# Optimization experiments

Hardware: AMD Instinct MI355X
Metric: run time of the kernel (lower is better)

## Reference

```python
import jax, jax.numpy as jnp
import numpy as np

B, SRC_LEN, TRG_LEN, DIM, H, D = 64, 500, 64, 512, 1024, 6
WIN = 2 * D + 1


def setup_inputs() -> dict:
    key = jax.random.key(0)
    ks = jax.random.split(key, 18)
    p = lambda k, shape: jax.random.normal(k, shape, dtype=jnp.float32) * 0.02
    return dict(
        src=jax.random.normal(ks[0], (B, SRC_LEN, DIM), dtype=jnp.float32),
        trg=jax.random.normal(ks[1], (B, TRG_LEN, DIM), dtype=jnp.float32),
        enc_Wih=p(ks[2], (3 * H, DIM)), enc_Whh=p(ks[3], (3 * H, H)),
        enc_bih=p(ks[4], (3 * H,)), enc_bhh=p(ks[5], (3 * H,)),
        dec_Wih=p(ks[6], (3 * H, DIM + H)), dec_Whh=p(ks[7], (3 * H, H)),
        dec_bih=p(ks[8], (3 * H,)), dec_bhh=p(ks[9], (3 * H,)),
        out_W=p(ks[10], (DIM, H)), out_b=p(ks[11], (DIM,)),
        ow_W=p(ks[12], (H, H)), ow_b=p(ks[13], (H,)),
        ov_W=p(ks[14], (1, H)), ov_b=p(ks[15], (1,)),
        attn_W=p(ks[16], (H, H)), attn_b=p(ks[17], (H,)),
    )


def _gru_cell(x, h, Wih, Whh, bih, bhh):
    # torch nn.GRU cell: r,z,n gate order
    gi = x @ Wih.T + bih
    gh = h @ Whh.T + bhh
    ir, iz, inn = jnp.split(gi, 3, axis=-1)
    hr, hz, hn = jnp.split(gh, 3, axis=-1)
    r = jax.nn.sigmoid(ir + hr)
    z = jax.nn.sigmoid(iz + hz)
    n = jnp.tanh(inn + r * hn)
    return (1.0 - z) * n + z * h


def reference(src, trg, enc_Wih, enc_Whh, enc_bih, enc_bhh,
              dec_Wih, dec_Whh, dec_bih, dec_bhh,
              out_W, out_b, ow_W, ow_b, ov_W, ov_b, attn_W, attn_b):
    b, L, dim = src.shape

    # ---- encoder GRU over time ----
    h0 = jnp.zeros((b, H), src.dtype)

    def enc_step(h, x_t):
        h = _gru_cell(x_t, h, enc_Wih, enc_Whh, enc_bih, enc_bhh)
        return h, h

    hT, enc_out = jax.lax.scan(enc_step, h0, jnp.swapaxes(src, 0, 1))
    enc_out = jnp.swapaxes(enc_out, 0, 1)  # [B, L, H]

    # ---- local attention (method='general') ----
    S = float(SRC_LEN - 2 * D - 1)
    sigma = D / 2.0
    offs = jnp.arange(-D, D + 1)

    def attention(s):  # s: [B, H]
        sig_inp = (jnp.tanh(s @ ow_W.T + ow_b) @ ov_W.T + ov_b)[:, 0]  # [B]
        pt = S * jax.nn.sigmoid(sig_inp) + D  # [B], in [D, L-D-1]
        center = jnp.floor(pt).astype(jnp.int32)  # int() trunc == floor (pt>0)
        idx = center[:, None] + offs[None, :]
        window = jnp.take_along_axis(enc_out, idx[:, :, None], axis=1)
        enc_w = window @ attn_W.T + attn_b  # general: attn(enc_output)
        alpha_hat = jnp.einsum('bwh,bh->bw', enc_w, s)
        gauss = jnp.exp(-((idx.astype(s.dtype) - pt[:, None]) ** 2) / (2.0 * sigma * sigma))
        alpha = jax.nn.softmax(alpha_hat * gauss, axis=1)
        return alpha, enc_w

    # teacher forcing (ratio=1.0): dec_input at step t is trg[:, t-1], zeros at t=0
    dec_inputs = jnp.concatenate(
        [jnp.zeros((b, 1, dim), src.dtype), trg[:, :-1, :]], axis=1)
    c0 = jnp.zeros((b, H), src.dtype)

    def dec_step(carry, x_t):
        h, c = carry
        rnn_in = jnp.concatenate([x_t, c], axis=1)  # [B, DIM+H]
        h = _gru_cell(rnn_in, h, dec_Wih, dec_Whh, dec_bih, dec_bhh)
        alpha, enc_w = attention(h)
        c = jnp.einsum('bw,bwh->bh', alpha, enc_w)  # attn context
        y = h @ out_W.T + out_b  # [B, DIM]
        return (h, c), y

    _, ys = jax.lax.scan(dec_step, (hT, c0), jnp.swapaxes(dec_inputs, 0, 1))
    return jnp.swapaxes(ys, 0, 1)  # [B, TRG_LEN, DIM]
```

## Files before the change

kernel.cpp:

```cpp
#include <hip/hip_runtime.h>


#define B_    64
#define SRCL  500
#define TRGL  64
#define DIM   512
#define H_    1024
#define WIN   13
#define DW    6

#define EWIHN 1572864
#define EWHHN 3145728
#define DWIHN 4718592
#define DWHHN 3145728
#define OUTWN 524288
#define OWWN  1048576
#define ATWN  1048576
#define BH    (B_ * H_)
#define HN    (2 * BH)
#define CN    BH
#define GBSTR 4096

typedef __attribute__((ext_vector_type(8)))  short short8;
typedef __attribute__((ext_vector_type(4)))  float floatx4;
typedef __attribute__((ext_vector_type(16))) float floatx16;

#define MFMA(a, b, c) __builtin_amdgcn_mfma_f32_32x32x16_bf16((a), (b), (c), 0, 0, 0)

__device__ __forceinline__ float bf2f(short s) {
  union { unsigned int u; float f; } v;
  v.u = ((unsigned int)(unsigned short)s) << 16;
  return v.f;
}
__device__ __forceinline__ short f2bf(float f) {
  union { float f; unsigned int u; } v;
  v.f = f;
  unsigned int u = v.u;
  u = (u + 0x7fffu + ((u >> 16) & 1u)) >> 16;
  return (short)u;
}
__device__ __forceinline__ floatx16 zero16() {
  floatx16 z;
#pragma unroll
  for (int i = 0; i < 16; ++i) z[i] = 0.f;
  return z;
}
__device__ __forceinline__ float sigm(float x) { return 1.f / (1.f + expf(-x)); }

__device__ __forceinline__ short8 load_c16(const short* p) {
  unsigned long long lo = __hip_atomic_load(
      (const unsigned long long*)p, __ATOMIC_RELAXED, __HIP_MEMORY_SCOPE_AGENT);
  unsigned long long hi = __hip_atomic_load(
      (const unsigned long long*)(p + 4), __ATOMIC_RELAXED,
      __HIP_MEMORY_SCOPE_AGENT);
  union { unsigned long long u[2]; short8 s; } x;
  x.u[0] = lo; x.u[1] = hi;
  return x.s;
}
__device__ __forceinline__ float load_c4f(const float* p) {
  unsigned int u = __hip_atomic_load((const unsigned int*)p, __ATOMIC_RELAXED,
                                     __HIP_MEMORY_SCOPE_AGENT);
  union { unsigned int u; float f; } x;
  x.u = u;
  return x.f;
}
__device__ __forceinline__ double load_c8d(const double* p) {
  unsigned long long u = __hip_atomic_load(
      (const unsigned long long*)p, __ATOMIC_RELAXED, __HIP_MEMORY_SCOPE_AGENT);
  union { unsigned long long u; double d; } x;
  x.u = u;
  return x.d;
}

__device__ __forceinline__ void store_c2(short* p, short v) {
  __hip_atomic_store((unsigned short*)p, (unsigned short)v, __ATOMIC_RELAXED,
                     __HIP_MEMORY_SCOPE_AGENT);
}
__device__ __forceinline__ void store_c4(float* p, float v) {
  __hip_atomic_store((unsigned int*)p, __float_as_uint(v), __ATOMIC_RELAXED,
                     __HIP_MEMORY_SCOPE_AGENT);
}
__device__ __forceinline__ void store_c8(double* p, double v) {
  union { double d; unsigned long long u; } x;
  x.d = v;
  __hip_atomic_store((unsigned long long*)p, x.u, __ATOMIC_RELAXED,
                     __HIP_MEMORY_SCOPE_AGENT);
}

__device__ __forceinline__ void split8(const float* p, short8& a0, short8& a1,
                                       short8& a2) {
  floatx4 v0 = *(const floatx4*)p;
  floatx4 v1 = *(const floatx4*)(p + 4);
  float vv[8];
#pragma unroll
  for (int j = 0; j < 4; ++j) { vv[j] = v0[j]; vv[4 + j] = v1[j]; }
#pragma unroll
  for (int j = 0; j < 8; ++j) {
    float v = vv[j];
    short s0 = f2bf(v);
    float r = v - bf2f(s0);
    short s1 = f2bf(r);
    r -= bf2f(s1);
    a0[j] = s0; a1[j] = s1; a2[j] = f2bf(r);
  }
}

__device__ __forceinline__ void publish_h(short* hw, int base, float hn) {
  short s0 = f2bf(hn);
  float rr = hn - bf2f(s0);
  short s1 = f2bf(rr);
  store_c2(hw + base, s0);
  store_c2(hw + HN + base, s1);
  store_c2(hw + 2 * HN + base, f2bf(rr - bf2f(s1)));
}

#define DECL6(P) floatx16 P##00 = zero16(), P##01 = zero16(), \
                          P##10 = zero16(), P##2 = zero16();
#define SUM6(P, r) (P##00[r] + P##01[r] + P##10[r] + P##2[r])

#define LOADA_C(a0v, a1v, a2v, ap, AN, kc)                                  \
  const short8 a0v = load_c16((ap) + (size_t)(kc)*16);                      \
  const short8 a1v = load_c16((ap) + (size_t)(AN) + (size_t)(kc)*16);       \
  const short8 a2v = load_c16((ap) + 2*(size_t)(AN) + (size_t)(kc)*16);

#define CHUNK6(P, a0v, a1v, a2v, bp, BN, kc)                                 \
  {                                                                          \
    const short8 b0v = *(const short8*)((bp) + (size_t)(kc)*16);             \
    const short8 b1v = *(const short8*)((bp) + (size_t)(BN) + (size_t)(kc)*16); \
    const short8 b2v = *(const short8*)((bp) + 2*(size_t)(BN) + (size_t)(kc)*16); \
    P##00 = MFMA(a0v, b0v, P##00);                                           \
    P##01 = MFMA(a0v, b1v, P##01);                                           \
    P##10 = MFMA(a1v, b0v, P##10);                                           \
    P##2  = MFMA(a0v, b2v, P##2);                                            \
    P##2  = MFMA(a1v, b1v, P##2);                                            \
    P##2  = MFMA(a2v, b0v, P##2);                                            \
  }

#define CHUNK6_NT(P, a0v, a1v, a2v, bp, BN, kc)                              \
  {                                                                          \
    const short8 b0v = __builtin_nontemporal_load(                           \
        (const short8*)((bp) + (size_t)(kc)*16));                            \
    const short8 b1v = __builtin_nontemporal_load(                           \
        (const short8*)((bp) + (size_t)(BN) + (size_t)(kc)*16));             \
    const short8 b2v = __builtin_nontemporal_load(                           \
        (const short8*)((bp) + 2*(size_t)(BN) + (size_t)(kc)*16));           \
    P##00 = MFMA(a0v, b0v, P##00);                                           \
    P##01 = MFMA(a0v, b1v, P##01);                                           \
    P##10 = MFMA(a1v, b0v, P##10);                                           \
    P##2  = MFMA(a0v, b2v, P##2);                                            \
    P##2  = MFMA(a1v, b1v, P##2);                                            \
    P##2  = MFMA(a2v, b0v, P##2);                                            \
  }

#define WRITE_TILE(dst, EXPR)                                        \
  do {                                                               \
    _Pragma("unroll") for (int r = 0; r < 16; ++r) {                 \
      int row_ = (r & 3) + 8 * (r >> 2) + 4 * (lane >> 5);           \
      (dst)[row_ * 32 + ra] = (EXPR);                                \
    }                                                                \
  } while (0)

__device__ __forceinline__ void group_barrier(int* flags, int fbase, int grp,
                                              int epoch, int tid) {
  asm volatile("s_waitcnt vmcnt(0) lgkmcnt(0)" ::: "memory");
  __syncthreads();
  if (tid == 0)
    __hip_atomic_store(&flags[fbase + grp], epoch, __ATOMIC_RELAXED,
                       __HIP_MEMORY_SCOPE_AGENT);
  if (tid < 128) {
    while (__hip_atomic_load(&flags[fbase + tid], __ATOMIC_RELAXED,
                             __HIP_MEMORY_SCOPE_AGENT) < epoch)
      __builtin_amdgcn_s_sleep(1);
  }
  __builtin_amdgcn_fence(__ATOMIC_ACQUIRE, "workgroup");
  __syncthreads();
}

__global__ void split3_kernel(const float* __restrict__ in,
                              short* __restrict__ out, int n) {
  const int i = blockIdx.x * 256 + threadIdx.x;
  if (i >= n) return;
  float v = in[i];
  short s0 = f2bf(v);
  float r = v - bf2f(s0);
  short s1 = f2bf(r);
  r -= bf2f(s1);
  out[i] = s0;
  out[n + i] = s1;
  out[2 * n + i] = f2bf(r);
}

__global__ __launch_bounds__(256) void enc_kernel(
    const float* __restrict__ src, const short* __restrict__ Wih,
    const short* __restrict__ Whh, const float* __restrict__ bih,
    const float* __restrict__ bhh, const short* __restrict__ attnW,
    const float* __restrict__ attn_b, float* __restrict__ h_f32,
    short* __restrict__ h_pl, float* __restrict__ enc_w,
    float* __restrict__ gb, int* __restrict__ flags) {
  const int tid  = threadIdx.x;
  const int lane = tid & 63;
  const int wid  = tid >> 6;
  const int ra   = lane & 31;
  const int koff = (lane >> 5) * 8;
  const int bid  = blockIdx.x;

  const bool isGRU = bid < 192;
  int mm, g, js, grp;
  if (isGRU) {
    mm = bid / 96; grp = bid % 96; g = grp >> 5; js = grp & 31;
  } else {
    int aux = bid - 192; mm = aux >> 5; js = aux & 31; g = 0; grp = 96 + js;
  }
  const int fbase = mm * 128;

  __shared__ float lds[8][1024];

  const int hrow = (mm * 32 + ra) * H_ + koff;
  const int nrow = g * H_ + js * 32 + ra;
  const short* wih_p = Wih + (size_t)nrow * DIM + koff;
  const short* whh_p = Whh + (size_t)nrow * H_ + koff;
  const short* atw_p = attnW + (size_t)(js * 32 + ra) * H_ + koff;
  const float* src_p = src + (size_t)(mm * 32 + ra) * (SRCL * DIM) + koff;

  int epoch = 0;
  for (int t = 0; t < SRCL; ++t) {
    const short* hp = h_pl + (t & 1) * BH + hrow;

    if (isGRU) {
      const float* xp = src_p + (size_t)t * DIM;
      if (g < 2) {
        DECL6(qa);
#pragma unroll 4
        for (int kc = wid * 8; kc < wid * 8 + 8; ++kc) {
          short8 a0v, a1v, a2v;
          split8(xp + kc * 16, a0v, a1v, a2v);
          CHUNK6(qa, a0v, a1v, a2v, wih_p, EWIHN, kc);
        }
#pragma unroll 4
        for (int kc = wid * 16; kc < wid * 16 + 16; ++kc) {
          LOADA_C(a0v, a1v, a2v, hp, HN, kc);
          CHUNK6(qa, a0v, a1v, a2v, whh_p, EWHHN, kc);
        }
        WRITE_TILE(lds[wid], SUM6(qa, r));
      } else {
        {
          DECL6(qa);
#pragma unroll 4
          for (int kc = wid * 8; kc < wid * 8 + 8; ++kc) {
            short8 a0v, a1v, a2v;
            split8(xp + kc * 16, a0v, a1v, a2v);
            CHUNK6(qa, a0v, a1v, a2v, wih_p, EWIHN, kc);
          }
          WRITE_TILE(lds[wid], SUM6(qa, r));
        }
        {
          DECL6(qb);
#pragma unroll 4
          for (int kc = wid * 16; kc < wid * 16 + 16; ++kc) {
            LOADA_C(a0v, a1v, a2v, hp, HN, kc);
            CHUNK6(qb, a0v, a1v, a2v, whh_p, EWHHN, kc);
          }
          WRITE_TILE(lds[4 + wid], SUM6(qb, r));
        }
      }
      __syncthreads();
      if (g < 2) {
        for (int idx = tid; idx < 1024; idx += 256) {
          const int bl = idx >> 5, j = idx & 31;
          float v = (lds[0][idx] + lds[1][idx]) + (lds[2][idx] + lds[3][idx]);
          store_c4(&gb[(size_t)(mm * 32 + bl) * GBSTR + g * 1024 + js * 32 + j], v);
        }
      } else {
        for (int idx = tid; idx < 1024; idx += 256) {
          const int bl = idx >> 5, j = idx & 31;
          float vi = (lds[0][idx] + lds[1][idx]) + (lds[2][idx] + lds[3][idx]);
          float vh = (lds[4][idx] + lds[5][idx]) + (lds[6][idx] + lds[7][idx]);
          store_c4(&gb[(size_t)(mm * 32 + bl) * GBSTR + 2 * 1024 + js * 32 + j], vi);
          store_c4(&gb[(size_t)(mm * 32 + bl) * GBSTR + 3 * 1024 + js * 32 + j], vh);
        }
      }
    } else if (t > 0) {
      if (wid < 3) {
        DECL6(qa);
        for (int kc = wid; kc < H_ / 16; kc += 3) {
          LOADA_C(a0v, a1v, a2v, hp, HN, kc);
          CHUNK6_NT(qa, a0v, a1v, a2v, atw_p, ATWN, kc);
        }
        WRITE_TILE(lds[wid], SUM6(qa, r));
      }
      __syncthreads();
      for (int idx = tid; idx < 1024; idx += 256) {
        const int bl = idx >> 5, j = idx & 31;
        float v = lds[0][idx] + lds[1][idx] + lds[2][idx] + attn_b[js * 32 + j];
        __builtin_nontemporal_store(
            v, &enc_w[((size_t)(mm * 32 + bl) * SRCL + (t - 1)) * H_ +
                      js * 32 + j]);
      }
    }
    group_barrier(flags, fbase, grp, ++epoch, tid);

    if (isGRU && grp < 32) {
      short* h0w = h_pl + ((t + 1) & 1) * BH;
      for (int idx = tid; idx < 1024; idx += 256) {
        const int bl = idx >> 5, j = idx & 31;
        const int jg = js * 32 + j;
        const int bg = mm * 32 + bl;
        float rv  = load_c4f(&gb[(size_t)bg * GBSTR + jg]);
        float zv  = load_c4f(&gb[(size_t)bg * GBSTR + 1024 + jg]);
        float niv = load_c4f(&gb[(size_t)bg * GBSTR + 2048 + jg]);
        float nhv = load_c4f(&gb[(size_t)bg * GBSTR + 3072 + jg]);
        float pr   = rv + bih[jg] + bhh[jg];
        float pz   = zv + bih[H_ + jg] + bhh[H_ + jg];
        float gi_n = niv + bih[2 * H_ + jg];
        float gh_n = nhv + bhh[2 * H_ + jg];
        float r_ = sigm(pr), z_ = sigm(pz);
        float n_ = tanhf(gi_n + r_ * gh_n);
        float ho = h_f32[bg * H_ + jg];
        float hn = (1.f - z_) * n_ + z_ * ho;
        h_f32[bg * H_ + jg] = hn;
        publish_h(h0w, bg * H_ + jg, hn);
      }
    }
    group_barrier(flags, fbase, grp, ++epoch, tid);
  }

  if (!isGRU) {
    const short* hp = h_pl + 0 * BH + hrow;
    if (wid < 3) {
      DECL6(qa);
      for (int kc = wid; kc < H_ / 16; kc += 3) {
        LOADA_C(a0v, a1v, a2v, hp, HN, kc);
        CHUNK6_NT(qa, a0v, a1v, a2v, atw_p, ATWN, kc);
      }
      WRITE_TILE(lds[wid], SUM6(qa, r));
    }
    __syncthreads();
    for (int idx = tid; idx < 1024; idx += 256) {
      const int bl = idx >> 5, j = idx & 31;
      float v = lds[0][idx] + lds[1][idx] + lds[2][idx] + attn_b[js * 32 + j];
      __builtin_nontemporal_store(
          v, &enc_w[((size_t)(mm * 32 + bl) * SRCL + (SRCL - 1)) * H_ +
                    js * 32 + j]);
    }
  }
}

__global__ __launch_bounds__(256) void dec_kernel(
    const float* __restrict__ trg, const short* __restrict__ Wih,
    const short* __restrict__ Whh, const float* __restrict__ bih,
    const float* __restrict__ bhh, const short* __restrict__ outW,
    const float* __restrict__ outb, const short* __restrict__ owW,
    const float* __restrict__ owb, const float* __restrict__ ovW,
    const float* __restrict__ ovb, const float* __restrict__ enc_w,
    float* __restrict__ h_f32, short* __restrict__ h_pl,
    short* __restrict__ c_pl, double* __restrict__ sig_part,
    float* __restrict__ gb, int* __restrict__ flags,
    float* __restrict__ out) {
  const int tid  = threadIdx.x;
  const int lane = tid & 63;
  const int wid  = tid >> 6;
  const int ra   = lane & 31;
  const int koff = (lane >> 5) * 8;
  const int bid  = blockIdx.x;

  const bool isGRU = bid < 192;
  int mm, g, js, grp;
  if (isGRU) {
    mm = bid / 96; grp = bid % 96; g = grp >> 5; js = grp & 31;
  } else {
    int aux = bid - 192; mm = aux >> 5; js = aux & 31; g = 0; grp = 96 + js;
  }
  const int fbase = mm * 128;

  __shared__ float lds[8][1024];
  __shared__ float al13[WIN];
  __shared__ float ah13[WIN];

  const int hrow = (mm * 32 + ra) * H_ + koff;
  const int nrow = g * H_ + js * 32 + ra;
  const short* wx_p = Wih + (size_t)nrow * (DIM + H_) + koff;
  const short* wc_p = wx_p + DIM;
  const short* wh_p = Whh + (size_t)nrow * H_ + koff;
  const float* trg_p = trg + (size_t)(mm * 32 + ra) * (TRGL * DIM) + koff;
  const short* cp = c_pl + hrow;
  const short* ow_p = owW + (size_t)(js * 32 + ra) * H_ + koff;
  const short* outw_p = outW + (size_t)((js & 15) * 32 + ra) * H_ + koff;
  const int b3 = mm * 32 + js;

  int epoch = 0;
  for (int t = 0; t < TRGL; ++t) {
    const int rd = t & 1, wr = (t + 1) & 1;
    const short* hp = h_pl + rd * BH + hrow;

    if (isGRU) {
      if (g < 2) {
        DECL6(qa);
        if (t > 0) {
          const float* xp = trg_p + (size_t)(t - 1) * DIM;
#pragma unroll 4
          for (int kc = wid * 8; kc < wid * 8 + 8; ++kc) {
            short8 a0v, a1v, a2v;
            split8(xp + kc * 16, a0v, a1v, a2v);
            CHUNK6(qa, a0v, a1v, a2v, wx_p, DWIHN, kc);
          }
        }
#pragma unroll 4
        for (int kc = wid * 16; kc < wid * 16 + 16; ++kc) {
          LOADA_C(a0v, a1v, a2v, cp, CN, kc);
          CHUNK6(qa, a0v, a1v, a2v, wc_p, DWIHN, kc);
        }
#pragma unroll 4
        for (int kc = wid * 16; kc < wid * 16 + 16; ++kc) {
          LOADA_C(a0v, a1v, a2v, hp, HN, kc);
          CHUNK6(qa, a0v, a1v, a2v, wh_p, DWHHN, kc);
        }
        WRITE_TILE(lds[wid], SUM6(qa, r));
      } else {
        {
          DECL6(qa);
          if (t > 0) {
            const float* xp = trg_p + (size_t)(t - 1) * DIM;
#pragma unroll 4
            for (int kc = wid * 8; kc < wid * 8 + 8; ++kc) {
              short8 a0v, a1v, a2v;
              split8(xp + kc * 16, a0v, a1v, a2v);
              CHUNK6(qa, a0v, a1v, a2v, wx_p, DWIHN, kc);
            }
          }
#pragma unroll 4
          for (int kc = wid * 16; kc < wid * 16 + 16; ++kc) {
            LOADA_C(a0v, a1v, a2v, cp, CN, kc);
            CHUNK6(qa, a0v, a1v, a2v, wc_p, DWIHN, kc);
          }
          WRITE_TILE(lds[wid], SUM6(qa, r));
        }
        {
          DECL6(qb);
#pragma unroll 4
          for (int kc = wid * 16; kc < wid * 16 + 16; ++kc) {
            LOADA_C(a0v, a1v, a2v, hp, HN, kc);
            CHUNK6(qb, a0v, a1v, a2v, wh_p, DWHHN, kc);
          }
          WRITE_TILE(lds[4 + wid], SUM6(qb, r));
        }
      }
      __syncthreads();
      if (g < 2) {
        for (int idx = tid; idx < 1024; idx += 256) {
          const int bl = idx >> 5, j = idx & 31;
          float v = (lds[0][idx] + lds[1][idx]) + (lds[2][idx] + lds[3][idx]);
          store_c4(&gb[(size_t)(mm * 32 + bl) * GBSTR + g * 1024 + js * 32 + j], v);
        }
      } else {
        for (int idx = tid; idx < 1024; idx += 256) {
          const int bl = idx >> 5, j = idx & 31;
          float vi = (lds[0][idx] + lds[1][idx]) + (lds[2][idx] + lds[3][idx]);
          float vh = (lds[4][idx] + lds[5][idx]) + (lds[6][idx] + lds[7][idx]);
          store_c4(&gb[(size_t)(mm * 32 + bl) * GBSTR + 2 * 1024 + js * 32 + j], vi);
          store_c4(&gb[(size_t)(mm * 32 + bl) * GBSTR + 3 * 1024 + js * 32 + j], vh);
        }
      }
    }
    group_barrier(flags, fbase, grp, ++epoch, tid);

    if (isGRU && grp < 32) {
      short* h0w = h_pl + wr * BH;
      for (int idx = tid; idx < 1024; idx += 256) {
        const int bl = idx >> 5, j = idx & 31;
        const int jg = js * 32 + j;
        const int bg = mm * 32 + bl;
        float rv  = load_c4f(&gb[(size_t)bg * GBSTR + jg]);
        float zv  = load_c4f(&gb[(size_t)bg * GBSTR + 1024 + jg]);
        float niv = load_c4f(&gb[(size_t)bg * GBSTR + 2048 + jg]);
        float nhv = load_c4f(&gb[(size_t)bg * GBSTR + 3072 + jg]);
        float pr   = rv + bih[jg] + bhh[jg];
        float pz   = zv + bih[H_ + jg] + bhh[H_ + jg];
        float gi_n = niv + bih[2 * H_ + jg];
        float gh_n = nhv + bhh[2 * H_ + jg];
        float r_ = sigm(pr), z_ = sigm(pz);
        float n_ = tanhf(gi_n + r_ * gh_n);
        float ho = load_c4f(&h_f32[bg * H_ + jg]);
        float hn = (1.f - z_) * n_ + z_ * ho;
        store_c4(&h_f32[bg * H_ + jg], hn);
        publish_h(h0w, bg * H_ + jg, hn);
      }
    }
    group_barrier(flags, fbase, grp, ++epoch, tid);

    const short* hc = h_pl + wr * BH + hrow;
    if (!isGRU) {
      if (wid < 3) {
        DECL6(qt);
        for (int kc = wid; kc < H_ / 16; kc += 3) {
          LOADA_C(a0v, a1v, a2v, hc, HN, kc);
          CHUNK6_NT(qt, a0v, a1v, a2v, ow_p, OWWN, kc);
        }
        WRITE_TILE(lds[wid], SUM6(qt, r));
      }
      __syncthreads();
      for (int idx = tid; idx < 1024; idx += 256) {
        float s3 = lds[0][idx] + lds[1][idx] + lds[2][idx] +
                   owb[js * 32 + (idx & 31)];
        lds[0][idx] = tanhf(s3);
      }
      __syncthreads();
      if (tid < 32) {
        double sv = 0.0;
#pragma unroll 8
        for (int j = 0; j < 32; ++j)
          sv += (double)lds[0][tid * 32 + j] * (double)ovW[js * 32 + j];
        store_c8(&sig_part[(size_t)(t * 32 + js) * B_ + mm * 32 + tid], sv);
      }
    } else if (g == 1 && js < 16) {
      if (wid < 3) {
        DECL6(qy);
        for (int kc = wid; kc < H_ / 16; kc += 3) {
          LOADA_C(a0v, a1v, a2v, hc, HN, kc);
          CHUNK6_NT(qy, a0v, a1v, a2v, outw_p, OUTWN, kc);
        }
        WRITE_TILE(lds[wid], SUM6(qy, r));
      }
      __syncthreads();
      for (int idx = tid; idx < 1024; idx += 256) {
        const int bl = idx >> 5, j = idx & 31;
        const int d = js * 32 + j;
        float v = lds[0][idx] + lds[1][idx] + lds[2][idx] + outb[d];
        __builtin_nontemporal_store(
            v, &out[(size_t)(mm * 32 + bl) * (TRGL * DIM) +
                    (size_t)t * DIM + d]);
      }
    }
    group_barrier(flags, fbase, grp, ++epoch, tid);

    if (!isGRU) {
      double sigv = (double)ovb[0];
      for (int p = 0; p < 32; ++p)
        sigv += load_c8d(&sig_part[(size_t)(t * 32 + p) * B_ + b3]);
      const double ptv = 487.0 / (1.0 + exp(-sigv)) + 6.0;
      const int center = (int)ptv;
      const int row0 = center - DW;
      const float ptf = (float)ptv;
      const float* s_vec = h_f32 + b3 * H_;
      if (wid < 3) {
        for (int w = wid; w < WIN; w += 3) {
          const float* ew =
              enc_w + ((size_t)b3 * SRCL + row0 + w) * H_ + lane * 16;
          float part = 0.f;
#pragma unroll
          for (int i = 0; i < 16; ++i)
            part += __builtin_nontemporal_load(&ew[i]) *
                    load_c4f(&s_vec[lane * 16 + i]);
#pragma unroll
          for (int off = 32; off; off >>= 1) part += __shfl_xor(part, off, 64);
          if (lane == 0) ah13[w] = part;
        }
      }
      __syncthreads();
      if (tid == 0) {
        float v[WIN], mx = -1e30f;
#pragma unroll
        for (int w = 0; w < WIN; ++w) {
          const float dd = (float)(row0 + w) - ptf;
          v[w] = ah13[w] * expf(-(dd * dd) / 18.f);
          mx = fmaxf(mx, v[w]);
        }
        float ssum = 0.f;
#pragma unroll
        for (int w = 0; w < WIN; ++w) { v[w] = expf(v[w] - mx); ssum += v[w]; }
        const float inv = 1.f / ssum;
#pragma unroll
        for (int w = 0; w < WIN; ++w) al13[w] = v[w] * inv;
      }
      __syncthreads();
      for (int hh = tid; hh < H_; hh += 256) {
        const float* ewb = enc_w + ((size_t)b3 * SRCL + row0) * H_ + hh;
        float acc = 0.f;
#pragma unroll
        for (int w = 0; w < WIN; ++w)
          acc += al13[w] * __builtin_nontemporal_load(&ewb[(size_t)w * H_]);
        short s0 = f2bf(acc);
        float rr = acc - bf2f(s0);
        short s1 = f2bf(rr);
        store_c2(&c_pl[b3 * H_ + hh], s0);
        store_c2(&c_pl[CN + b3 * H_ + hh], s1);
        store_c2(&c_pl[2 * CN + b3 * H_ + hh], f2bf(rr - bf2f(s1)));
      }
    }
    group_barrier(flags, fbase, grp, ++epoch, tid);
  }
}

extern "C" void kernel_launch(void* const* d_in, const int* in_sizes, int n_in,
                              void* d_out, int out_size, void* d_ws,
                              size_t ws_size, hipStream_t stream) {
  (void)in_sizes; (void)n_in; (void)out_size; (void)ws_size;

  const float* src     = (const float*)d_in[0];
  const float* trg     = (const float*)d_in[1];
  const float* enc_Wih = (const float*)d_in[2];
  const float* enc_Whh = (const float*)d_in[3];
  const float* enc_bih = (const float*)d_in[4];
  const float* enc_bhh = (const float*)d_in[5];
  const float* dec_Wih = (const float*)d_in[6];
  const float* dec_Whh = (const float*)d_in[7];
  const float* dec_bih = (const float*)d_in[8];
  const float* dec_bhh = (const float*)d_in[9];
  const float* out_W   = (const float*)d_in[10];
  const float* out_b   = (const float*)d_in[11];
  const float* ow_W    = (const float*)d_in[12];
  const float* ow_b    = (const float*)d_in[13];
  const float* ov_W    = (const float*)d_in[14];
  const float* ov_b    = (const float*)d_in[15];
  const float* attn_W  = (const float*)d_in[16];
  const float* attn_b  = (const float*)d_in[17];

  char* ws = (char*)d_ws;
  size_t off = 0;
  auto take = [&](size_t bytes) {
    size_t o = off;
    off += (bytes + 255) & ~(size_t)255;
    return o;
  };

  float* h_f32   = (float*)(ws + take(BH * 4));
  short* h_pl    = (short*)(ws + take((size_t)3 * HN * 2));
  short* c_pl    = (short*)(ws + take((size_t)3 * CN * 2));
  int*   flags_e = (int*)(ws + take(256 * 4));
  int*   flags_d = (int*)(ws + take(256 * 4));
  const size_t zero_bytes = off;

  double* sig_part = (double*)(ws + take((size_t)TRGL * 32 * B_ * 8));
  float* gate_buf  = (float*)(ws + take((size_t)B_ * GBSTR * 4));
  short* pWihE = (short*)(ws + take((size_t)3 * EWIHN * 2));
  short* pWhhE = (short*)(ws + take((size_t)3 * EWHHN * 2));
  short* pWihD = (short*)(ws + take((size_t)3 * DWIHN * 2));
  short* pWhhD = (short*)(ws + take((size_t)3 * DWHHN * 2));
  short* pOutW = (short*)(ws + take((size_t)3 * OUTWN * 2));
  short* pOwW  = (short*)(ws + take((size_t)3 * OWWN * 2));
  short* pAtW  = (short*)(ws + take((size_t)3 * ATWN * 2));
  float* enc_w = (float*)(ws + take((size_t)B_ * SRCL * H_ * 4));

  hipMemsetAsync(ws, 0, zero_bytes, stream);

  auto split = [&](const float* in, short* outp, int n) {
    split3_kernel<<<dim3((n + 255) / 256), dim3(256), 0, stream>>>(in, outp, n);
  };
  split(enc_Wih, pWihE, EWIHN);
  split(enc_Whh, pWhhE, EWHHN);
  split(dec_Wih, pWihD, DWIHN);
  split(dec_Whh, pWhhD, DWHHN);
  split(out_W,  pOutW, OUTWN);
  split(ow_W,   pOwW,  OWWN);
  split(attn_W, pAtW,  ATWN);

  enc_kernel<<<dim3(256), dim3(256), 0, stream>>>(
      src, pWihE, pWhhE, enc_bih, enc_bhh, pAtW, attn_b, h_f32, h_pl, enc_w,
      gate_buf, flags_e);

  dec_kernel<<<dim3(256), dim3(256), 0, stream>>>(
      trg, pWihD, pWhhD, dec_bih, dec_bhh, pOutW, out_b, pOwW, ow_b, ov_W,
      ov_b, enc_w, h_f32, h_pl, c_pl, sig_part, gate_buf, flags_d,
      (float*)d_out);
}
```

Before: 28.66 ms.

## Repartition encoder GRU blocks by K-slice across all three gates

Result: slower. 31.61 ms (+10.3%).

```diff
diff --git a/kernel.cpp b/kernel.cpp
--- a/kernel.cpp
+++ b/kernel.cpp
@@ -57,6 +57,16 @@
   x.u[0] = lo; x.u[1] = hi;
   return x.s;
 }
+__device__ __forceinline__ floatx4 load_c16f(const float* p) {
+  unsigned long long lo = __hip_atomic_load(
+      (const unsigned long long*)p, __ATOMIC_RELAXED, __HIP_MEMORY_SCOPE_AGENT);
+  unsigned long long hi = __hip_atomic_load(
+      (const unsigned long long*)(p + 2), __ATOMIC_RELAXED,
+      __HIP_MEMORY_SCOPE_AGENT);
+  union { unsigned long long u[2]; floatx4 f; } x;
+  x.u[0] = lo; x.u[1] = hi;
+  return x.f;
+}
 __device__ __forceinline__ float load_c4f(const float* p) {
   unsigned int u = __hip_atomic_load((const unsigned int*)p, __ATOMIC_RELAXED,
                                      __HIP_MEMORY_SCOPE_AGENT);
@@ -87,10 +97,10 @@
                      __HIP_MEMORY_SCOPE_AGENT);
 }
 
-__device__ __forceinline__ void split8(const float* p, short8& a0, short8& a1,
-                                       short8& a2) {
-  floatx4 v0 = *(const floatx4*)p;
-  floatx4 v1 = *(const floatx4*)(p + 4);
+__device__ __forceinline__ void split8_nt(const float* p, short8& a0,
+                                          short8& a1, short8& a2) {
+  floatx4 v0 = __builtin_nontemporal_load((const floatx4*)p);
+  floatx4 v1 = __builtin_nontemporal_load((const floatx4*)(p + 4));
   float vv[8];
 #pragma unroll
   for (int j = 0; j < 4; ++j) { vv[j] = v0[j]; vv[4 + j] = v1[j]; }
@@ -196,7 +206,7 @@
     const float* __restrict__ bhh, const short* __restrict__ attnW,
     const float* __restrict__ attn_b, float* __restrict__ h_f32,
     short* __restrict__ h_pl, float* __restrict__ enc_w,
-    float* __restrict__ gb, int* __restrict__ flags) {
+    float* __restrict__ gb2, int* __restrict__ flags) {
   const int tid  = threadIdx.x;
   const int lane = tid & 63;
   const int wid  = tid >> 6;
@@ -205,21 +215,42 @@
   const int bid  = blockIdx.x;
 
   const bool isGRU = bid < 192;
-  int mm, g, js, grp;
+  int mm, js, slice, grp;
   if (isGRU) {
-    mm = bid / 96; grp = bid % 96; g = grp >> 5; js = grp & 31;
+    slice = bid / 64;
+    const int rem = bid % 64;
+    mm = rem >> 5; js = rem & 31;
+    grp = slice * 32 + js;
   } else {
-    int aux = bid - 192; mm = aux >> 5; js = aux & 31; g = 0; grp = 96 + js;
+    const int aux = bid - 192;
+    mm = aux >> 5; js = aux & 31; slice = 0; grp = 96 + js;
   }
   const int fbase = mm * 128;
 
-  __shared__ float lds[8][1024];
+  __shared__ float lds[12][1024];
 
   const int hrow = (mm * 32 + ra) * H_ + koff;
-  const int nrow = g * H_ + js * 32 + ra;
-  const short* wih_p = Wih + (size_t)nrow * DIM + koff;
-  const short* whh_p = Whh + (size_t)nrow * H_ + koff;
-  const short* atw_p = attnW + (size_t)(js * 32 + ra) * H_ + koff;
+  const short* bp0;
+  const short* bp1;
+  const short* bp2;
+  size_t BNv;
+  int kbase;
+  if (isGRU) {
+    if (slice == 0) {
+      bp0 = Wih + (size_t)(0 * H_ + js * 32 + ra) * DIM + koff;
+      bp1 = Wih + (size_t)(1 * H_ + js * 32 + ra) * DIM + koff;
+      bp2 = Wih + (size_t)(2 * H_ + js * 32 + ra) * DIM + koff;
+      BNv = EWIHN; kbase = wid * 8;
+    } else {
+      bp0 = Whh + (size_t)(0 * H_ + js * 32 + ra) * H_ + koff;
+      bp1 = Whh + (size_t)(1 * H_ + js * 32 + ra) * H_ + koff;
+      bp2 = Whh + (size_t)(2 * H_ + js * 32 + ra) * H_ + koff;
+      BNv = EWHHN; kbase = (slice - 1) * 32 + wid * 8;
+    }
+  } else {
+    bp0 = bp1 = bp2 = attnW + (size_t)(js * 32 + ra) * H_ + koff;
+    BNv = ATWN; kbase = 0;
+  }
   const float* src_p = src + (size_t)(mm * 32 + ra) * (SRCL * DIM) + koff;
 
   int epoch = 0;
@@ -227,56 +258,53 @@
     const short* hp = h_pl + (t & 1) * BH + hrow;
 
     if (isGRU) {
-      const float* xp = src_p + (size_t)t * DIM;
-      if (g < 2) {
+      short8 A0[8], A1[8], A2[8];
+      if (slice == 0) {
+        const float* xp = src_p + (size_t)t * DIM;
+#pragma unroll
+        for (int k8 = 0; k8 < 8; ++k8)
+          split8_nt(xp + (size_t)(wid * 8 + k8) * 16, A0[k8], A1[k8], A2[k8]);
+      } else {
+#pragma unroll
+        for (int k8 = 0; k8 < 8; ++k8) {
+          const int kcg = kbase + k8;
+          A0[k8] = load_c16(hp + (size_t)kcg * 16);
+          A1[k8] = load_c16(hp + (size_t)HN + (size_t)kcg * 16);
+          A2[k8] = load_c16(hp + 2 * (size_t)HN + (size_t)kcg * 16);
+        }
+      }
+      {
         DECL6(qa);
-#pragma unroll 4
-        for (int kc = wid * 8; kc < wid * 8 + 8; ++kc) {
-          short8 a0v, a1v, a2v;
-          split8(xp + kc * 16, a0v, a1v, a2v);
-          CHUNK6(qa, a0v, a1v, a2v, wih_p, EWIHN, kc);
-        }
-#pragma unroll 4
-        for (int kc = wid * 16; kc < wid * 16 + 16; ++kc) {
-          LOADA_C(a0v, a1v, a2v, hp, HN, kc);
-          CHUNK6(qa, a0v, a1v, a2v, whh_p, EWHHN, kc);
-        }
-        WRITE_TILE(lds[wid], SUM6(qa, r));
-      } else {
-        {
-          DECL6(qa);
-#pragma unroll 4
-          for (int kc = wid * 8; kc < wid * 8 + 8; ++kc) {
-            short8 a0v, a1v, a2v;
-            split8(xp + kc * 16, a0v, a1v, a2v);
-            CHUNK6(qa, a0v, a1v, a2v, wih_p, EWIHN, kc);
-          }
-          WRITE_TILE(lds[wid], SUM6(qa, r));
-        }
-        {
-          DECL6(qb);
-#pragma unroll 4
-          for (int kc = wid * 16; kc < wid * 16 + 16; ++kc) {
-            LOADA_C(a0v, a1v, a2v, hp, HN, kc);
-            CHUNK6(qb, a0v, a1v, a2v, whh_p, EWHHN, kc);
-          }
-          WRITE_TILE(lds[4 + wid], SUM6(qb, r));
-        }
-      }
-      __syncthreads();
-      if (g < 2) {
-        for (int idx = tid; idx < 1024; idx += 256) {
-          const int bl = idx >> 5, j = idx & 31;
-          float v = (lds[0][idx] + lds[1][idx]) + (lds[2][idx] + lds[3][idx]);
-          store_c4(&gb[(size_t)(mm * 32 + bl) * GBSTR + g * 1024 + js * 32 + j], v);
-        }
-      } else {
-        for (int idx = tid; idx < 1024; idx += 256) {
-          const int bl = idx >> 5, j = idx & 31;
-          float vi = (lds[0][idx] + lds[1][idx]) + (lds[2][idx] + lds[3][idx]);
-          float vh = (lds[4][idx] + lds[5][idx]) + (lds[6][idx] + lds[7][idx]);
-          store_c4(&gb[(size_t)(mm * 32 + bl) * GBSTR + 2 * 1024 + js * 32 + j], vi);
-          store_c4(&gb[(size_t)(mm * 32 + bl) * GBSTR + 3 * 1024 + js * 32 + j], vh);
+#pragma unroll
+        for (int k8 = 0; k8 < 8; ++k8)
+          CHUNK6(qa, A0[k8], A1[k8], A2[k8], bp0, BNv, kbase + k8);
+        WRITE_TILE(lds[0 * 4 + wid], SUM6(qa, r));
+      }
+      {
+        DECL6(qa);
+#pragma unroll
+        for (int k8 = 0; k8 < 8; ++k8)
+          CHUNK6(qa, A0[k8], A1[k8], A2[k8], bp1, BNv, kbase + k8);
+        WRITE_TILE(lds[1 * 4 + wid], SUM6(qa, r));
+      }
+      {
+        DECL6(qa);
+#pragma unroll
+        for (int k8 = 0; k8 < 8; ++k8)
+          CHUNK6(qa, A0[k8], A1[k8], A2[k8], bp2, BNv, kbase + k8);
+        WRITE_TILE(lds[2 * 4 + wid], SUM6(qa, r));
+      }
+      __syncthreads();
+      for (int idx = tid; idx < 1024; idx += 256) {
+        const int bl = idx >> 5, j = idx & 31;
+        const int bg = mm * 32 + bl;
+        const int col = js * 32 + j;
+        float* gp = gb2 + ((size_t)bg * 1024 + col) * 12 + slice;
+#pragma unroll
+        for (int g = 0; g < 3; ++g) {
+          float v = (lds[g * 4 + 0][idx] + lds[g * 4 + 1][idx]) +
+                    (lds[g * 4 + 2][idx] + lds[g * 4 + 3][idx]);
+          store_c4(gp + g * 4, v);
         }
       }
     } else if (t > 0) {
@@ -284,7 +312,7 @@
         DECL6(qa);
         for (int kc = wid; kc < H_ / 16; kc += 3) {
           LOADA_C(a0v, a1v, a2v, hp, HN, kc);
-          CHUNK6_NT(qa, a0v, a1v, a2v, atw_p, ATWN, kc);
+          CHUNK6_NT(qa, a0v, a1v, a2v, bp0, ATWN, kc);
         }
         WRITE_TILE(lds[wid], SUM6(qa, r));
       }
@@ -299,20 +327,20 @@
     }
     group_barrier(flags, fbase, grp, ++epoch, tid);
 
-    if (isGRU && grp < 32) {
+    if (isGRU && slice == 0) {
       short* h0w = h_pl + ((t + 1) & 1) * BH;
       for (int idx = tid; idx < 1024; idx += 256) {
         const int bl = idx >> 5, j = idx & 31;
         const int jg = js * 32 + j;
         const int bg = mm * 32 + bl;
-        float rv  = load_c4f(&gb[(size_t)bg * GBSTR + jg]);
-        float zv  = load_c4f(&gb[(size_t)bg * GBSTR + 1024 + jg]);
-        float niv = load_c4f(&gb[(size_t)bg * GBSTR + 2048 + jg]);
-        float nhv = load_c4f(&gb[(size_t)bg * GBSTR + 3072 + jg]);
-        float pr   = rv + bih[jg] + bhh[jg];
-        float pz   = zv + bih[H_ + jg] + bhh[H_ + jg];
-        float gi_n = niv + bih[2 * H_ + jg];
-        float gh_n = nhv + bhh[2 * H_ + jg];
+        const float* gp = gb2 + ((size_t)bg * 1024 + jg) * 12;
+        floatx4 qr = load_c16f(gp);
+        floatx4 qz = load_c16f(gp + 4);
+        floatx4 qn = load_c16f(gp + 8);
+        float pr   = ((qr[0] + qr[1]) + qr[2]) + bih[jg] + bhh[jg];
+        float pz   = ((qz[0] + qz[1]) + qz[2]) + bih[H_ + jg] + bhh[H_ + jg];
+        float gi_n = qn[0] + bih[2 * H_ + jg];
+        float gh_n = (qn[1] + qn[2]) + bhh[2 * H_ + jg];
         float r_ = sigm(pr), z_ = sigm(pz);
         float n_ = tanhf(gi_n + r_ * gh_n);
         float ho = h_f32[bg * H_ + jg];
@@ -330,7 +358,7 @@
       DECL6(qa);
       for (int kc = wid; kc < H_ / 16; kc += 3) {
         LOADA_C(a0v, a1v, a2v, hp, HN, kc);
-        CHUNK6_NT(qa, a0v, a1v, a2v, atw_p, ATWN, kc);
+        CHUNK6_NT(qa, a0v, a1v, a2v, bp0, ATWN, kc);
       }
       WRITE_TILE(lds[wid], SUM6(qa, r));
     }
@@ -400,7 +428,7 @@
 #pragma unroll 4
           for (int kc = wid * 8; kc < wid * 8 + 8; ++kc) {
             short8 a0v, a1v, a2v;
-            split8(xp + kc * 16, a0v, a1v, a2v);
+            split8_nt(xp + kc * 16, a0v, a1v, a2v);
             CHUNK6(qa, a0v, a1v, a2v, wx_p, DWIHN, kc);
           }
         }
@@ -423,7 +451,7 @@
 #pragma unroll 4
             for (int kc = wid * 8; kc < wid * 8 + 8; ++kc) {
               short8 a0v, a1v, a2v;
-              split8(xp + kc * 16, a0v, a1v, a2v);
+              split8_nt(xp + kc * 16, a0v, a1v, a2v);
               CHUNK6(qa, a0v, a1v, a2v, wx_p, DWIHN, kc);
             }
           }
@@ -631,6 +659,7 @@
 
   double* sig_part = (double*)(ws + take((size_t)TRGL * 32 * B_ * 8));
   float* gate_buf  = (float*)(ws + take((size_t)B_ * GBSTR * 4));
+  float* gb2       = (float*)(ws + take((size_t)B_ * 1024 * 12 * 4));
   short* pWihE = (short*)(ws + take((size_t)3 * EWIHN * 2));
   short* pWhhE = (short*)(ws + take((size_t)3 * EWHHN * 2));
   short* pWihD = (short*)(ws + take((size_t)3 * DWIHN * 2));
@@ -655,7 +684,7 @@
 
   enc_kernel<<<dim3(256), dim3(256), 0, stream>>>(
       src, pWihE, pWhhE, enc_bih, enc_bhh, pAtW, attn_b, h_f32, h_pl, enc_w,
-      gate_buf, flags_e);
+      gb2, flags_e);
 
   dec_kernel<<<dim3(256), dim3(256), 0, stream>>>(
       trg, pWihD, pWhhD, dec_bih, dec_bhh, pOutW, out_b, pOwW, ow_b, ov_W,
```
